# Kernel optimization log

Hardware: AMD Instinct MI355X
Metric: run time of the kernel (lower is better)

## Reference

```python
import jax, jax.numpy as jnp
import numpy as np

N_NODES = 100000
N_EDGES = 1600000
D_FEAT = 512
HEADS = 8
UNITS1 = 8          # layer1: 8 heads x 8 units, concat -> 64
HIDDEN = HEADS * UNITS1
OUT_DIM = 16        # layer2: 8 heads x 16 units, avg -> 16
N_IDX = 10000
NEG_SLOPE = 0.2     # LeakyReLU slope used by GAT attention


def _gat_layer(x, edges, W, a_src, a_dst, merge):
    """One multi-head GAT layer.
    x: [N, F], edges: [E, 2] with (dst, src) columns,
    W: [F, H, U], a_src/a_dst: [H, U].
    """
    n = x.shape[0]
    dst = edges[:, 0]
    src = edges[:, 1]
    h = jnp.einsum('nf,fhu->nhu', x, W)                      # [N, H, U]
    # per-node attention score halves, then gather per edge (cheaper than
    # gathering full features first)
    s_src = jnp.einsum('nhu,hu->nh', h, a_src)               # [N, H]
    s_dst = jnp.einsum('nhu,hu->nh', h, a_dst)               # [N, H]
    e = s_dst[dst] + s_src[src]                              # [E, H]
    e = jnp.where(e > 0, e, NEG_SLOPE * e)                   # LeakyReLU
    # segment softmax over incoming edges of each dst node (stable)
    m = jax.ops.segment_max(e, dst, num_segments=n)          # [N, H]
    m = jnp.where(jnp.isfinite(m), m, 0.0)                   # empty segments
    ex = jnp.exp(e - m[dst])                                 # [E, H]
    denom = jax.ops.segment_sum(ex, dst, num_segments=n)     # [N, H]
    alpha = ex / jnp.maximum(denom[dst], 1e-9)               # [E, H]
    msg = h[src] * alpha[:, :, None]                         # [E, H, U]
    out = jax.ops.segment_sum(msg, dst, num_segments=n)      # [N, H, U]
    if merge == 'concat':
        return out.reshape(n, -1)                            # [N, H*U]
    return out.mean(axis=1)                                  # [N, U]


def setup_inputs() -> dict:
    key = jax.random.key(0)
    ks = jax.random.split(key, 9)
    node_states = jax.random.normal(ks[0], (N_NODES, D_FEAT), dtype=jnp.float32)
    edges = jax.random.randint(ks[1], (N_EDGES, 2), 0, N_NODES, dtype=jnp.int32).astype(jnp.int64)
    indices = jax.random.randint(ks[2], (N_IDX,), 0, N_NODES, dtype=jnp.int32).astype(jnp.int64)
    W1 = jax.random.normal(ks[3], (D_FEAT, HEADS, UNITS1), dtype=jnp.float32) / np.sqrt(D_FEAT)
    a1_src = jax.random.normal(ks[4], (HEADS, UNITS1), dtype=jnp.float32) / np.sqrt(UNITS1)
    a1_dst = jax.random.normal(ks[5], (HEADS, UNITS1), dtype=jnp.float32) / np.sqrt(UNITS1)
    W2 = jax.random.normal(ks[6], (HIDDEN, HEADS, OUT_DIM), dtype=jnp.float32) / np.sqrt(HIDDEN)
    a2_src = jax.random.normal(ks[7], (HEADS, OUT_DIM), dtype=jnp.float32) / np.sqrt(OUT_DIM)
    a2_dst = jax.random.normal(ks[8], (HEADS, OUT_DIM), dtype=jnp.float32) / np.sqrt(OUT_DIM)
    return {
        'node_states': node_states, 'edges': edges, 'indices': indices,
        'W1': W1, 'a1_src': a1_src, 'a1_dst': a1_dst,
        'W2': W2, 'a2_src': a2_src, 'a2_dst': a2_dst,
    }


def reference(node_states, edges, indices, W1, a1_src, a1_dst, W2, a2_src, a2_dst):
    # layer 1: concat merge + ELU nonlinearity (standard GAT hidden layer)
    x = _gat_layer(node_states, edges, W1, a1_src, a1_dst, merge='concat')
    x = jax.nn.elu(x)                                        # [N, 64]
    # layer 2: average merge, linear output logits
    out = _gat_layer(x, edges, W2, a2_src, a2_dst, merge='avg')  # [N, OUT_DIM]
    return jnp.take(out, indices, axis=0)                    # [N_IDX, OUT_DIM]
```

## Files before the change

kernel.cpp:

```cpp
#include <hip/hip_runtime.h>
#include <hip/hip_bf16.h>

#define NN 100000
#define NE 1600000
#define DF 512
#define NIDX 10000

#define NBKT 512
#define BKT_W 196
#define EDGES_PER_BKT_BLK 3125

typedef __attribute__((ext_vector_type(8))) short short8v;
typedef __attribute__((ext_vector_type(4))) float float4v;

__device__ __forceinline__ float eluf(float x) { return x > 0.f ? x : expm1f(x); }
__device__ __forceinline__ float lrelu(float x) { return x > 0.f ? x : 0.2f * x; }
__device__ __forceinline__ ushort f2bf(float f) {
  __hip_bfloat16 b = __float2bfloat16(f);
  return *(ushort*)&b;
}

__device__ __forceinline__ void glds16(const void* gsrc, void* ldst) {
  __builtin_amdgcn_global_load_lds(
      (const __attribute__((address_space(1))) uint32_t*)(uintptr_t)gsrc,
      (__attribute__((address_space(3))) uint32_t*)(uintptr_t)ldst, 16, 0, 0);
}

__global__ __launch_bounds__(256) void prep_w_kernel(const float* __restrict__ W1,
                                                     ushort* __restrict__ Wt_hi, ushort* __restrict__ Wt_lo,
                                                     int* __restrict__ bkt_cnt) {
  if (blockIdx.x == 0) {
    bkt_cnt[threadIdx.x] = 0;
    bkt_cnt[threadIdx.x + 256] = 0;
  }
  int t = blockIdx.x * 256 + threadIdx.x;
  if (t >= DF * 64) return;
  int k = t >> 6, n = t & 63;
  float w = W1[t];
  ushort hi = f2bf(w);
  __hip_bfloat16 hb = *(__hip_bfloat16*)&hi;
  ushort lo = f2bf(w - __bfloat162float(hb));
  Wt_hi[(size_t)n * DF + k] = hi;
  Wt_lo[(size_t)n * DF + k] = lo;
}

#define BSTRIDE 40
__global__ __launch_bounds__(256) void gemm1_mfma(const float* __restrict__ x,
                                                  const ushort* __restrict__ Wt_hi, const ushort* __restrict__ Wt_lo,
                                                  const float* __restrict__ a1s, const float* __restrict__ a1d,
                                                  ushort* __restrict__ h1b, float* __restrict__ s_src,
                                                  float* __restrict__ s_dst) {
  __shared__ __align__(16) char smem[53248];
  float* Abuf[2];
  Abuf[0] = (float*)smem;
  Abuf[1] = (float*)(smem + 16384);
  ushort* Bhi[2]; ushort* Blo[2];
  Bhi[0] = (ushort*)(smem + 32768);
  Blo[0] = Bhi[0] + 64 * BSTRIDE;
  Bhi[1] = Blo[0] + 64 * BSTRIDE;
  Blo[1] = Bhi[1] + 64 * BSTRIDE;
  float* Cs = (float*)smem;

  const int tid = threadIdx.x;
  const int mb = blockIdx.x * 128;
  const int wave = tid >> 6, l = tid & 63;
  const int wm = wave * 32;
  const int lm = l & 15, kq = l >> 4, kg = kq * 8;

  float4v acc[2][4];
#pragma unroll
  for (int i = 0; i < 2; ++i)
#pragma unroll
    for (int j = 0; j < 4; ++j) acc[i][j] = (float4v){0.f, 0.f, 0.f, 0.f};

  size_t asrc[4];
#pragma unroll
  for (int i = 0; i < 4; ++i) {
    int g = mb + wm + 8 * i + (l >> 3);
    if (g > NN - 1) g = NN - 1;
    asrc[i] = (size_t)g * DF + (l & 7) * 4;
  }
  const int bn = tid & 63, bk = (tid >> 6) * 8;

#pragma unroll
  for (int i = 0; i < 4; ++i)
    glds16(x + asrc[i], (char*)Abuf[0] + wave * 4096 + i * 1024);
  {
    uint4 rbh = *(const uint4*)&Wt_hi[(size_t)bn * DF + bk];
    uint4 rbl = *(const uint4*)&Wt_lo[(size_t)bn * DF + bk];
    *(uint4*)&Bhi[0][bn * BSTRIDE + bk] = rbh;
    *(uint4*)&Blo[0][bn * BSTRIDE + bk] = rbl;
  }
  __syncthreads();

  for (int ks = 0; ks < 16; ++ks) {
    const int k0 = ks * 32;
    const int cur = ks & 1;
    if (ks < 15) {
#pragma unroll
      for (int i = 0; i < 4; ++i)
        glds16(x + asrc[i] + k0 + 32, (char*)Abuf[cur ^ 1] + wave * 4096 + i * 1024);
    }
    uint4 rbh, rbl;
    if (ks < 15) {
      rbh = *(const uint4*)&Wt_hi[(size_t)bn * DF + k0 + 32 + bk];
      rbl = *(const uint4*)&Wt_lo[(size_t)bn * DF + k0 + 32 + bk];
    }
    short8v ah[2], al[2];
#pragma unroll
    for (int mt = 0; mt < 2; ++mt) {
      const float* p = Abuf[cur] + wave * 1024 + (mt * 16 + lm) * 32 + kg;
      float4 f0 = *(const float4*)p;
      float4 f1 = *(const float4*)(p + 4);
      float f[8] = {f0.x, f0.y, f0.z, f0.w, f1.x, f1.y, f1.z, f1.w};
#pragma unroll
      for (int c = 0; c < 8; ++c) {
        uint u = __float_as_uint(f[c]);
        ah[mt][c] = (short)(u >> 16);
        float hf = __uint_as_float(u & 0xFFFF0000u);
        al[mt][c] = (short)(__float_as_uint(f[c] - hf) >> 16);
      }
    }
    short8v bh[4], bl[4];
#pragma unroll
    for (int nt = 0; nt < 4; ++nt) {
      bh[nt] = *(const short8v*)&Bhi[cur][(nt * 16 + lm) * BSTRIDE + kg];
      bl[nt] = *(const short8v*)&Blo[cur][(nt * 16 + lm) * BSTRIDE + kg];
    }
#pragma unroll
    for (int mt = 0; mt < 2; ++mt)
#pragma unroll
      for (int nt = 0; nt < 4; ++nt) {
        acc[mt][nt] = __builtin_amdgcn_mfma_f32_16x16x32_bf16(ah[mt], bh[nt], acc[mt][nt], 0, 0, 0);
        acc[mt][nt] = __builtin_amdgcn_mfma_f32_16x16x32_bf16(ah[mt], bl[nt], acc[mt][nt], 0, 0, 0);
        acc[mt][nt] = __builtin_amdgcn_mfma_f32_16x16x32_bf16(al[mt], bh[nt], acc[mt][nt], 0, 0, 0);
      }
    if (ks < 15) {
      *(uint4*)&Bhi[cur ^ 1][bn * BSTRIDE + bk] = rbh;
      *(uint4*)&Blo[cur ^ 1][bn * BSTRIDE + bk] = rbl;
    }
    __syncthreads();
  }

#pragma unroll
  for (int mt = 0; mt < 2; ++mt)
#pragma unroll
    for (int nt = 0; nt < 4; ++nt)
#pragma unroll
      for (int r = 0; r < 4; ++r)
        Cs[(wm + mt * 16 + kq * 4 + r) * 65 + nt * 16 + lm] = acc[mt][nt][r];
  __syncthreads();

  {
    int row = tid >> 1, c0 = (tid & 1) * 32;
    int g = mb + row;
    if (g < NN) {
      uint u[16];
#pragma unroll
      for (int j = 0; j < 16; ++j) {
        uint p0 = f2bf(Cs[row * 65 + c0 + 2 * j]);
        uint p1 = f2bf(Cs[row * 65 + c0 + 2 * j + 1]);
        u[j] = p0 | (p1 << 16);
      }
#pragma unroll
      for (int q = 0; q < 4; ++q)
        *(uint4*)&h1b[(size_t)g * 64 + c0 + 8 * q] = *(uint4*)&u[4 * q];
      int half = tid & 1;
      float4 ssv, ddv;
      float* ssp = &ssv.x;
      float* ddp = &ddv.x;
#pragma unroll
      for (int hq = 0; hq < 4; ++hq) {
        int hh = half * 4 + hq;
        float ss = 0.f, dd = 0.f;
#pragma unroll
        for (int u8 = 0; u8 < 8; ++u8) {
          float hv = Cs[row * 65 + hh * 8 + u8];
          ss = fmaf(hv, a1s[hh * 8 + u8], ss);
          dd = fmaf(hv, a1d[hh * 8 + u8], dd);
        }
        ssp[hq] = ss; ddp[hq] = dd;
      }
      *(float4*)&s_src[(size_t)g * 8 + half * 4] = ssv;
      *(float4*)&s_dst[(size_t)g * 8 + half * 4] = ddv;
    }
  }
}

__global__ __launch_bounds__(256) void gemm2_fused(const float* __restrict__ A, const float* __restrict__ B,
                                                   __hip_bfloat162* __restrict__ Cb,
                                                   const float* __restrict__ a2s, const float* __restrict__ a2d,
                                                   float* __restrict__ s_src, float* __restrict__ s_dst,
                                                   int M, int N, int K) {
  __shared__ float sm[2 * 32 * 68];
  float* As = sm;
  float* Bs = sm + 32 * 68;
  float* Cs = sm;
  const int tid = threadIdx.x;
  const int m0 = blockIdx.x * 64;
  const int n0 = blockIdx.y * 64;
  const int tx = tid & 15, ty = tid >> 4;
  float acc[4][4] = {};
  for (int k0 = 0; k0 < K; k0 += 32) {
    for (int j = tid; j < 512; j += 256) {
      int r = j >> 3, kq = j & 7;
      int row = m0 + r;
      float4 v = make_float4(0.f, 0.f, 0.f, 0.f);
      if (row < M) v = *(const float4*)&A[(size_t)row * K + k0 + kq * 4];
      v.x = eluf(v.x); v.y = eluf(v.y); v.z = eluf(v.z); v.w = eluf(v.w);
      As[(kq * 4 + 0) * 68 + r] = v.x; As[(kq * 4 + 1) * 68 + r] = v.y;
      As[(kq * 4 + 2) * 68 + r] = v.z; As[(kq * 4 + 3) * 68 + r] = v.w;
    }
    for (int j = tid; j < 512; j += 256) {
      int kr = j >> 4, nq = j & 15;
      *(float4*)&Bs[kr * 68 + nq * 4] = *(const float4*)&B[(size_t)(k0 + kr) * N + n0 + nq * 4];
    }
    __syncthreads();
#pragma unroll
    for (int kk = 0; kk < 32; ++kk) {
      float4 a4 = *(const float4*)&As[kk * 68 + ty * 4];
      float4 b4 = *(const float4*)&Bs[kk * 68 + tx * 4];
      float av[4] = {a4.x, a4.y, a4.z, a4.w};
      float bv[4] = {b4.x, b4.y, b4.z, b4.w};
#pragma unroll
      for (int i = 0; i < 4; ++i)
#pragma unroll
        for (int jj = 0; jj < 4; ++jj)
          acc[i][jj] = fmaf(av[i], bv[jj], acc[i][jj]);
    }
    __syncthreads();
  }
#pragma unroll
  for (int i = 0; i < 4; ++i) {
    int row = m0 + ty * 4 + i;
    if (row < M) {
      __hip_bfloat162 p0, p1;
      p0.x = __float2bfloat16(acc[i][0]); p0.y = __float2bfloat16(acc[i][1]);
      p1.x = __float2bfloat16(acc[i][2]); p1.y = __float2bfloat16(acc[i][3]);
      size_t base = ((size_t)row * N + n0 + tx * 4) >> 1;
      Cb[base] = p0; Cb[base + 1] = p1;
    }
#pragma unroll
    for (int jj = 0; jj < 4; ++jj)
      Cs[(ty * 4 + i) * 65 + tx * 4 + jj] = acc[i][jj];
  }
  __syncthreads();
  {
    int row = tid >> 2, q = tid & 3;
    int g = m0 + row;
    if (g < M) {
      int hh = (n0 >> 4) + q;
      float ss = 0.f, dd = 0.f;
#pragma unroll
      for (int u = 0; u < 16; ++u) {
        float v = Cs[row * 65 + q * 16 + u];
        ss = fmaf(v, a2s[hh * 16 + u], ss);
        dd = fmaf(v, a2d[hh * 16 + u], dd);
      }
      s_src[(size_t)g * 8 + hh] = ss;
      s_dst[(size_t)g * 8 + hh] = dd;
    }
  }
}

__global__ __launch_bounds__(256) void bkt_hist_kernel(const int2* __restrict__ edges, int* __restrict__ bkt_cnt) {
  __shared__ int h[NBKT];
  const int tid = threadIdx.x;
  h[tid] = 0; h[tid + 256] = 0;
  __syncthreads();
  const int i0 = blockIdx.x * EDGES_PER_BKT_BLK;
  const int i1 = min(i0 + EDGES_PER_BKT_BLK, NE);
  for (int i = i0 + tid; i < i1; i += 256) atomicAdd(&h[edges[i].x / BKT_W], 1);
  __syncthreads();
  if (h[tid]) atomicAdd(&bkt_cnt[tid], h[tid]);
  if (h[tid + 256]) atomicAdd(&bkt_cnt[tid + 256], h[tid + 256]);
}

__global__ __launch_bounds__(NBKT) void bkt_scan_kernel(const int* __restrict__ bkt_cnt, int* __restrict__ bkt_base,
                                                        int* __restrict__ bkt_cursor, int* __restrict__ row_off) {
  __shared__ int s[NBKT];
  int tid = threadIdx.x;
  int v = bkt_cnt[tid];
  s[tid] = v;
  __syncthreads();
  for (int off = 1; off < NBKT; off <<= 1) {
    int t = (tid >= off) ? s[tid - off] : 0;
    __syncthreads();
    s[tid] += t;
    __syncthreads();
  }
  int excl = s[tid] - v;
  bkt_base[tid] = excl;
  bkt_cursor[tid] = excl;
  if (tid == NBKT - 1) bkt_base[NBKT] = s[tid];
  if (tid == 0) row_off[NN] = NE;
}

__global__ __launch_bounds__(256) void bkt_reorder_kernel(const int2* __restrict__ edges, int* __restrict__ bkt_cursor,
                                                          uint* __restrict__ pairs) {
  __shared__ int h[NBKT];
  __shared__ int lbase[NBKT];
  __shared__ int cur[NBKT];
  const int tid = threadIdx.x;
  h[tid] = 0; h[tid + 256] = 0;
  __syncthreads();
  const int i0 = blockIdx.x * EDGES_PER_BKT_BLK;
  const int i1 = min(i0 + EDGES_PER_BKT_BLK, NE);
  for (int i = i0 + tid; i < i1; i += 256) atomicAdd(&h[edges[i].x / BKT_W], 1);
  __syncthreads();
#pragma unroll
  for (int q = 0; q < 2; ++q) {
    int b = tid + q * 256;
    int c = h[b];
    lbase[b] = c ? atomicAdd(&bkt_cursor[b], c) : 0;
    cur[b] = 0;
  }
  __syncthreads();
  for (int i = i0 + tid; i < i1; i += 256) {
    int2 e = edges[i];
    int bk = e.x / BKT_W;
    int r = atomicAdd(&cur[bk], 1);
    pairs[lbase[bk] + r] = ((uint)(e.x - bk * BKT_W) << 24) | (uint)e.y;
  }
}

__global__ __launch_bounds__(256) void bkt_build_kernel(const uint* __restrict__ pairs, const int* __restrict__ bkt_base,
                                                        int* __restrict__ row_off, int* __restrict__ ssrc) {
  __shared__ int hist[256];
  __shared__ int ts[256];
  __shared__ int cur[256];
  const int b = blockIdx.x, tid = threadIdx.x;
  const int d0 = b * BKT_W;
  if (d0 >= NN) return;
  const int nd = min(BKT_W, NN - d0);
  const int beg = bkt_base[b], end = bkt_base[b + 1];
  hist[tid] = 0;
  __syncthreads();
  for (int i = beg + tid; i < end; i += 256) atomicAdd(&hist[pairs[i] >> 24], 1);
  __syncthreads();
  int v = hist[tid];
  ts[tid] = v;
  __syncthreads();
  for (int off = 1; off < 256; off <<= 1) {
    int t = (tid >= off) ? ts[tid - off] : 0;
    __syncthreads();
    ts[tid] += t;
    __syncthreads();
  }
  int excl = ts[tid] - v;
  if (tid < nd) row_off[d0 + tid] = beg + excl;
  cur[tid] = beg + excl;
  __syncthreads();
  for (int i = beg + tid; i < end; i += 256) {
    uint p = pairs[i];
    int pos = atomicAdd(&cur[p >> 24], 1);
    ssrc[pos] = (int)(p & 0xFFFFFFu);
  }
}

__global__ __launch_bounds__(256) void agg1_kernel(const int* __restrict__ row_off, const int* __restrict__ srcs,
                                                   const float* __restrict__ s_src, const float* __restrict__ s_dst,
                                                   const __hip_bfloat16* __restrict__ hb, float* __restrict__ out, int n) {
  int wave = (blockIdx.x * 256 + threadIdx.x) >> 6;
  int lane = threadIdx.x & 63;
  if (wave >= n) return;
  int hh = lane >> 3;
  float sd = s_dst[(size_t)wave * 8 + hh];
  int beg = row_off[wave], end = row_off[wave + 1];
  float acc = 0.f, den = 0.f;
  int i = beg;
  for (; i + 8 <= end; i += 8) {
    int s[8];
#pragma unroll
    for (int j = 0; j < 8; ++j) s[j] = srcs[i + j];
    float e[8], hv[8];
#pragma unroll
    for (int j = 0; j < 8; ++j) e[j] = s_src[(size_t)s[j] * 8 + hh];
#pragma unroll
    for (int j = 0; j < 8; ++j) hv[j] = __bfloat162float(hb[(size_t)s[j] * 64 + lane]);
#pragma unroll
    for (int j = 0; j < 8; ++j) {
      float xj = __expf(lrelu(sd + e[j]));
      den += xj;
      acc = fmaf(xj, hv[j], acc);
    }
  }
  for (; i < end; ++i) {
    int s0 = srcs[i];
    float x0 = __expf(lrelu(sd + s_src[(size_t)s0 * 8 + hh]));
    den += x0;
    acc = fmaf(x0, __bfloat162float(hb[(size_t)s0 * 64 + lane]), acc);
  }
  out[(size_t)wave * 64 + lane] = acc / fmaxf(den, 1e-9f);
}

__global__ __launch_bounds__(256) void agg2_idx_kernel(const int* __restrict__ row_off, const int* __restrict__ srcs,
                                                       const float* __restrict__ s_src, const float* __restrict__ s_dst,
                                                       const __hip_bfloat162* __restrict__ h2b, const int* __restrict__ idx,
                                                       float* __restrict__ out, int ni) {
  int w = (blockIdx.x * 256 + threadIdx.x) >> 6;
  int lane = threadIdx.x & 63;
  if (w >= ni) return;
  int node = idx[w];
  int hh = lane >> 3, o2 = lane & 7;
  float sd = s_dst[(size_t)node * 8 + hh];
  int beg = row_off[node], end = row_off[node + 1];
  float a0 = 0.f, a1 = 0.f, den = 0.f;
  int i = beg;
  for (; i + 4 <= end; i += 4) {
    int s0 = srcs[i], s1 = srcs[i + 1], s2 = srcs[i + 2], s3 = srcs[i + 3];
    float e0 = s_src[(size_t)s0 * 8 + hh];
    float e1 = s_src[(size_t)s1 * 8 + hh];
    float e2 = s_src[(size_t)s2 * 8 + hh];
    float e3 = s_src[(size_t)s3 * 8 + hh];
    float2 v0 = __bfloat1622float2(h2b[(size_t)s0 * 64 + hh * 8 + o2]);
    float2 v1 = __bfloat1622float2(h2b[(size_t)s1 * 64 + hh * 8 + o2]);
    float2 v2 = __bfloat1622float2(h2b[(size_t)s2 * 64 + hh * 8 + o2]);
    float2 v3 = __bfloat1622float2(h2b[(size_t)s3 * 64 + hh * 8 + o2]);
    float x0 = __expf(lrelu(sd + e0));
    float x1 = __expf(lrelu(sd + e1));
    float x2 = __expf(lrelu(sd + e2));
    float x3 = __expf(lrelu(sd + e3));
    den += (x0 + x1) + (x2 + x3);
    a0 = fmaf(x0, v0.x, fmaf(x1, v1.x, fmaf(x2, v2.x, fmaf(x3, v3.x, a0))));
    a1 = fmaf(x0, v0.y, fmaf(x1, v1.y, fmaf(x2, v2.y, fmaf(x3, v3.y, a1))));
  }
  for (; i < end; ++i) {
    int s0 = srcs[i];
    float x0 = __expf(lrelu(sd + s_src[(size_t)s0 * 8 + hh]));
    float2 v0 = __bfloat1622float2(h2b[(size_t)s0 * 64 + hh * 8 + o2]);
    den += x0;
    a0 = fmaf(x0, v0.x, a0);
    a1 = fmaf(x0, v0.y, a1);
  }
  float r0 = a0 / fmaxf(den, 1e-9f);
  float r1 = a1 / fmaxf(den, 1e-9f);
  for (int m = 8; m < 64; m <<= 1) {
    r0 += __shfl_xor(r0, m, 64);
    r1 += __shfl_xor(r1, m, 64);
  }
  if (lane < 8) {
    float2 wv = make_float2(r0 * 0.125f, r1 * 0.125f);
    *(float2*)&out[(size_t)w * 16 + lane * 2] = wv;
  }
}

extern "C" void kernel_launch(void* const* d_in, const int* in_sizes, int n_in,
                              void* d_out, int out_size, void* d_ws, size_t ws_size,
                              hipStream_t stream) {
  const float* x   = (const float*)d_in[0];
  const int2* edges = (const int2*)d_in[1];
  const int* indices = (const int*)d_in[2];
  const float* W1  = (const float*)d_in[3];
  const float* a1s = (const float*)d_in[4];
  const float* a1d = (const float*)d_in[5];
  const float* W2  = (const float*)d_in[6];
  const float* a2s = (const float*)d_in[7];
  const float* a2d = (const float*)d_in[8];
  float* out = (float*)d_out;

  char* ws = (char*)d_ws;
  size_t off = 0;
  auto alloc = [&](size_t bytes) {
    void* p = ws + off;
    off = (off + bytes + 255) & ~(size_t)255;
    return p;
  };
  float* s1src = (float*)alloc((size_t)NN * 8 * 4);
  float* s1dst = (float*)alloc((size_t)NN * 8 * 4);
  float* out1  = (float*)alloc((size_t)NN * 64 * 4);
  ushort* h1b  = (ushort*)alloc((size_t)NN * 64 * 2);
  __hip_bfloat162* h2b = (__hip_bfloat162*)alloc((size_t)NN * 128 * 2);
  int* row_off = (int*)alloc(((size_t)NN + 1) * 4);
  int* ssrc    = (int*)alloc((size_t)NE * 4);
  uint* pairs  = (uint*)alloc((size_t)NE * 4);
  ushort* Wt_hi = (ushort*)alloc((size_t)DF * 64 * 2);
  ushort* Wt_lo = (ushort*)alloc((size_t)DF * 64 * 2);
  int* bkt_cnt    = (int*)alloc(NBKT * 4);
  int* bkt_base   = (int*)alloc((NBKT + 1) * 4);
  int* bkt_cursor = (int*)alloc(NBKT * 4);

  dim3 b256(256);
  prep_w_kernel<<<dim3((DF * 64 + 255) / 256), b256, 0, stream>>>(W1, Wt_hi, Wt_lo, bkt_cnt);
  gemm1_mfma<<<dim3((NN + 127) / 128), b256, 0, stream>>>(x, Wt_hi, Wt_lo, a1s, a1d, h1b, s1src, s1dst);
  bkt_hist_kernel<<<dim3(NBKT), b256, 0, stream>>>(edges, bkt_cnt);
  bkt_scan_kernel<<<dim3(1), dim3(NBKT), 0, stream>>>(bkt_cnt, bkt_base, bkt_cursor, row_off);
  bkt_reorder_kernel<<<dim3(NBKT), b256, 0, stream>>>(edges, bkt_cursor, pairs);
  bkt_build_kernel<<<dim3(NBKT), b256, 0, stream>>>(pairs, bkt_base, row_off, ssrc);
  agg1_kernel<<<dim3(NN / 4), b256, 0, stream>>>(row_off, ssrc, s1src, s1dst, (const __hip_bfloat16*)h1b, out1, NN);
  gemm2_fused<<<dim3((NN + 63) / 64, 2), b256, 0, stream>>>(out1, W2, h2b, a2s, a2d, s1src, s1dst, NN, 128, 64);
  agg2_idx_kernel<<<dim3((NIDX * 64 + 255) / 256), b256, 0, stream>>>(row_off, ssrc, s1src, s1dst, h2b, indices, out, NIDX);
}
```

Baseline: 267.1 us.

## Merge edge histogram into gemm1 launch and widen gemm2 tile to all columns

The bucket histogram now runs as extra blocks inside the gemm1 launch. This removes one kernel launch and lets the histogram overlap with the layer-1 GEMM. gemm2 now computes all 128 output columns per block instead of splitting them across two grid columns, so the ELU-transformed A tile is loaded once. The attention scores are computed in registers with a lane shuffle instead of a shared-memory pass. The risks are higher register use per thread in gemm2 and a larger shared-memory footprint for the histogram blocks, which reuse gemm1's 52KB allocation and may lower occupancy.

```diff
diff --git a/kernel.cpp b/kernel.cpp
--- a/kernel.cpp
+++ b/kernel.cpp
@@ -9,6 +9,7 @@
 #define NBKT 512
 #define BKT_W 196
 #define EDGES_PER_BKT_BLK 3125
+#define GEMM1_NB 782
 
 typedef __attribute__((ext_vector_type(8))) short short8v;
 typedef __attribute__((ext_vector_type(4))) float float4v;
@@ -45,12 +46,29 @@
 }
 
 #define BSTRIDE 40
-__global__ __launch_bounds__(256) void gemm1_mfma(const float* __restrict__ x,
+__global__ __launch_bounds__(256) void gemm1_hist(const float* __restrict__ x,
                                                   const ushort* __restrict__ Wt_hi, const ushort* __restrict__ Wt_lo,
                                                   const float* __restrict__ a1s, const float* __restrict__ a1d,
                                                   ushort* __restrict__ h1b, float* __restrict__ s_src,
-                                                  float* __restrict__ s_dst) {
+                                                  float* __restrict__ s_dst,
+                                                  const int2* __restrict__ edges, int* __restrict__ bkt_cnt) {
   __shared__ __align__(16) char smem[53248];
+  const int tid = threadIdx.x;
+
+  if (blockIdx.x >= GEMM1_NB) {
+    int* h = (int*)smem;
+    h[tid] = 0; h[tid + 256] = 0;
+    __syncthreads();
+    const int b = blockIdx.x - GEMM1_NB;
+    const int i0 = b * EDGES_PER_BKT_BLK;
+    const int i1 = min(i0 + EDGES_PER_BKT_BLK, NE);
+    for (int i = i0 + tid; i < i1; i += 256) atomicAdd(&h[edges[i].x / BKT_W], 1);
+    __syncthreads();
+    if (h[tid]) atomicAdd(&bkt_cnt[tid], h[tid]);
+    if (h[tid + 256]) atomicAdd(&bkt_cnt[tid + 256], h[tid + 256]);
+    return;
+  }
+
   float* Abuf[2];
   Abuf[0] = (float*)smem;
   Abuf[1] = (float*)(smem + 16384);
@@ -61,7 +79,6 @@
   Blo[1] = Bhi[1] + 64 * BSTRIDE;
   float* Cs = (float*)smem;
 
-  const int tid = threadIdx.x;
   const int mb = blockIdx.x * 128;
   const int wave = tid >> 6, l = tid & 63;
   const int wm = wave * 32;
@@ -191,89 +208,68 @@
                                                    __hip_bfloat162* __restrict__ Cb,
                                                    const float* __restrict__ a2s, const float* __restrict__ a2d,
                                                    float* __restrict__ s_src, float* __restrict__ s_dst,
-                                                   int M, int N, int K) {
-  __shared__ float sm[2 * 32 * 68];
+                                                   int M) {
+  __shared__ float sm[6528];
   float* As = sm;
   float* Bs = sm + 32 * 68;
-  float* Cs = sm;
   const int tid = threadIdx.x;
   const int m0 = blockIdx.x * 64;
-  const int n0 = blockIdx.y * 64;
   const int tx = tid & 15, ty = tid >> 4;
-  float acc[4][4] = {};
-  for (int k0 = 0; k0 < K; k0 += 32) {
+  float acc[4][8] = {};
+  for (int k0 = 0; k0 < 64; k0 += 32) {
     for (int j = tid; j < 512; j += 256) {
       int r = j >> 3, kq = j & 7;
       int row = m0 + r;
       float4 v = make_float4(0.f, 0.f, 0.f, 0.f);
-      if (row < M) v = *(const float4*)&A[(size_t)row * K + k0 + kq * 4];
+      if (row < M) v = *(const float4*)&A[(size_t)row * 64 + k0 + kq * 4];
       v.x = eluf(v.x); v.y = eluf(v.y); v.z = eluf(v.z); v.w = eluf(v.w);
       As[(kq * 4 + 0) * 68 + r] = v.x; As[(kq * 4 + 1) * 68 + r] = v.y;
       As[(kq * 4 + 2) * 68 + r] = v.z; As[(kq * 4 + 3) * 68 + r] = v.w;
     }
-    for (int j = tid; j < 512; j += 256) {
-      int kr = j >> 4, nq = j & 15;
-      *(float4*)&Bs[kr * 68 + nq * 4] = *(const float4*)&B[(size_t)(k0 + kr) * N + n0 + nq * 4];
+    for (int j = tid; j < 1024; j += 256) {
+      int kr = j >> 5, nq = j & 31;
+      *(float4*)&Bs[kr * 136 + nq * 4] = *(const float4*)&B[(size_t)(k0 + kr) * 128 + nq * 4];
     }
     __syncthreads();
 #pragma unroll
     for (int kk = 0; kk < 32; ++kk) {
       float4 a4 = *(const float4*)&As[kk * 68 + ty * 4];
-      float4 b4 = *(const float4*)&Bs[kk * 68 + tx * 4];
+      float4 b0 = *(const float4*)&Bs[kk * 136 + tx * 8];
+      float4 b1 = *(const float4*)&Bs[kk * 136 + tx * 8 + 4];
       float av[4] = {a4.x, a4.y, a4.z, a4.w};
-      float bv[4] = {b4.x, b4.y, b4.z, b4.w};
+      float bv[8] = {b0.x, b0.y, b0.z, b0.w, b1.x, b1.y, b1.z, b1.w};
 #pragma unroll
       for (int i = 0; i < 4; ++i)
 #pragma unroll
-        for (int jj = 0; jj < 4; ++jj)
+        for (int jj = 0; jj < 8; ++jj)
           acc[i][jj] = fmaf(av[i], bv[jj], acc[i][jj]);
     }
     __syncthreads();
   }
+  const int hx = tx >> 1, half8 = (tx & 1) * 8;
 #pragma unroll
   for (int i = 0; i < 4; ++i) {
     int row = m0 + ty * 4 + i;
+    float ss = 0.f, dd = 0.f;
+#pragma unroll
+    for (int c = 0; c < 8; ++c) {
+      ss = fmaf(acc[i][c], a2s[hx * 16 + half8 + c], ss);
+      dd = fmaf(acc[i][c], a2d[hx * 16 + half8 + c], dd);
+    }
+    ss += __shfl_xor(ss, 1, 64);
+    dd += __shfl_xor(dd, 1, 64);
     if (row < M) {
-      __hip_bfloat162 p0, p1;
-      p0.x = __float2bfloat16(acc[i][0]); p0.y = __float2bfloat16(acc[i][1]);
-      p1.x = __float2bfloat16(acc[i][2]); p1.y = __float2bfloat16(acc[i][3]);
-      size_t base = ((size_t)row * N + n0 + tx * 4) >> 1;
-      Cb[base] = p0; Cb[base + 1] = p1;
-    }
-#pragma unroll
-    for (int jj = 0; jj < 4; ++jj)
-      Cs[(ty * 4 + i) * 65 + tx * 4 + jj] = acc[i][jj];
-  }
-  __syncthreads();
-  {
-    int row = tid >> 2, q = tid & 3;
-    int g = m0 + row;
-    if (g < M) {
-      int hh = (n0 >> 4) + q;
-      float ss = 0.f, dd = 0.f;
-#pragma unroll
-      for (int u = 0; u < 16; ++u) {
-        float v = Cs[row * 65 + q * 16 + u];
-        ss = fmaf(v, a2s[hh * 16 + u], ss);
-        dd = fmaf(v, a2d[hh * 16 + u], dd);
+      uint u[4];
+#pragma unroll
+      for (int q = 0; q < 4; ++q)
+        u[q] = (uint)f2bf(acc[i][2 * q]) | ((uint)f2bf(acc[i][2 * q + 1]) << 16);
+      *(uint4*)&Cb[(size_t)row * 64 + tx * 4] = *(uint4*)u;
+      if ((tx & 1) == 0) {
+        s_src[(size_t)row * 8 + hx] = ss;
+        s_dst[(size_t)row * 8 + hx] = dd;
       }
-      s_src[(size_t)g * 8 + hh] = ss;
-      s_dst[(size_t)g * 8 + hh] = dd;
-    }
-  }
-}
-
-__global__ __launch_bounds__(256) void bkt_hist_kernel(const int2* __restrict__ edges, int* __restrict__ bkt_cnt) {
-  __shared__ int h[NBKT];
-  const int tid = threadIdx.x;
-  h[tid] = 0; h[tid + 256] = 0;
-  __syncthreads();
-  const int i0 = blockIdx.x * EDGES_PER_BKT_BLK;
-  const int i1 = min(i0 + EDGES_PER_BKT_BLK, NE);
-  for (int i = i0 + tid; i < i1; i += 256) atomicAdd(&h[edges[i].x / BKT_W], 1);
-  __syncthreads();
-  if (h[tid]) atomicAdd(&bkt_cnt[tid], h[tid]);
-  if (h[tid + 256]) atomicAdd(&bkt_cnt[tid + 256], h[tid + 256]);
+    }
+  }
 }
 
 __global__ __launch_bounds__(NBKT) void bkt_scan_kernel(const int* __restrict__ bkt_cnt, int* __restrict__ bkt_base,
@@ -482,12 +478,12 @@
 
   dim3 b256(256);
   prep_w_kernel<<<dim3((DF * 64 + 255) / 256), b256, 0, stream>>>(W1, Wt_hi, Wt_lo, bkt_cnt);
-  gemm1_mfma<<<dim3((NN + 127) / 128), b256, 0, stream>>>(x, Wt_hi, Wt_lo, a1s, a1d, h1b, s1src, s1dst);
-  bkt_hist_kernel<<<dim3(NBKT), b256, 0, stream>>>(edges, bkt_cnt);
+  gemm1_hist<<<dim3(GEMM1_NB + NBKT), b256, 0, stream>>>(x, Wt_hi, Wt_lo, a1s, a1d, h1b, s1src, s1dst,
+                                                          edges, bkt_cnt);
   bkt_scan_kernel<<<dim3(1), dim3(NBKT), 0, stream>>>(bkt_cnt, bkt_base, bkt_cursor, row_off);
   bkt_reorder_kernel<<<dim3(NBKT), b256, 0, stream>>>(edges, bkt_cursor, pairs);
   bkt_build_kernel<<<dim3(NBKT), b256, 0, stream>>>(pairs, bkt_base, row_off, ssrc);
   agg1_kernel<<<dim3(NN / 4), b256, 0, stream>>>(row_off, ssrc, s1src, s1dst, (const __hip_bfloat16*)h1b, out1, NN);
-  gemm2_fused<<<dim3((NN + 63) / 64, 2), b256, 0, stream>>>(out1, W2, h2b, a2s, a2d, s1src, s1dst, NN, 128, 64);
+  gemm2_fused<<<dim3((NN + 63) / 64), b256, 0, stream>>>(out1, W2, h2b, a2s, a2d, s1src, s1dst, NN);
   agg2_idx_kernel<<<dim3((NIDX * 64 + 255) / 256), b256, 0, stream>>>(row_off, ssrc, s1src, s1dst, h2b, indices, out, NIDX);
 }
```

Measured after the change: 254.9 us. -4.5%, faster.
